# Kernel optimization log

Measured on AMD Instinct MI355X. Metric: run time of the kernel, lower is better.

Reference implementation:

```python
import jax, jax.numpy as jnp
import numpy as np

N = 100000   # nodes
E = 3200000  # edges (avg degree 32)
IN = 128     # in_channels
H = 128      # hidden_channels
G = 512      # graphs in batch


def setup_inputs() -> dict:
    key = jax.random.key(0)
    ks = jax.random.split(key, 8)
    x = jax.random.normal(ks[0], (N, IN), dtype=jnp.float32)
    edge_index = jax.random.randint(ks[1], (2, E), 0, N, dtype=jnp.int64)
    batch = jnp.sort(jax.random.randint(ks[2], (N,), 0, G, dtype=jnp.int64))
    s_in = 1.0 / np.sqrt(IN)
    s_h = 1.0 / np.sqrt(H)
    W1 = jax.random.normal(ks[3], (IN, H), dtype=jnp.float32) * s_in
    b1 = jnp.zeros((H,), dtype=jnp.float32)
    W2 = jax.random.normal(ks[4], (H, H), dtype=jnp.float32) * s_h
    b2 = jnp.zeros((H,), dtype=jnp.float32)
    Wc = jax.random.normal(ks[5], (H, 1), dtype=jnp.float32) * s_h
    bc = jnp.zeros((1,), dtype=jnp.float32)
    return {"x": x, "edge_index": edge_index, "batch": batch,
            "W1": W1, "b1": b1, "W2": W2, "b2": b2, "Wc": Wc, "bc": bc}


def _gcn_conv(x, W, b, src, dst, n):
    # PyG GCNConv: x' = D^{-1/2} (A+I) D^{-1/2} X W + b  (self-loops already in src/dst)
    h = x @ W                                      # [n, H] small GEMM
    ones = jnp.ones(src.shape[0], dtype=h.dtype)
    deg = jax.ops.segment_sum(ones, dst, num_segments=n)
    dinv = jnp.where(deg > 0, jax.lax.rsqrt(deg), 0.0)
    norm = dinv[src] * dinv[dst]                   # [E+n]
    msgs = h[src] * norm[:, None]                  # gather + scale (memory-bound)
    return jax.ops.segment_sum(msgs, dst, num_segments=n) + b


def reference(x, edge_index, batch, W1, b1, W2, b2, Wc, bc):
    n = x.shape[0]
    loop = jnp.arange(n, dtype=edge_index.dtype)
    src = jnp.concatenate([edge_index[0], loop])   # add self-loops
    dst = jnp.concatenate([edge_index[1], loop])
    h = jax.nn.relu(_gcn_conv(x, W1, b1, src, dst, n))
    h = jax.nn.relu(_gcn_conv(h, W2, b2, src, dst, n))
    # global_mean_pool: segment mean over graph ids
    counts = jax.ops.segment_sum(jnp.ones(n, dtype=h.dtype), batch, num_segments=G)
    sums = jax.ops.segment_sum(h, batch, num_segments=G)
    pooled = sums / jnp.maximum(counts, 1.0)[:, None]   # [G, H]
    return jax.nn.sigmoid(pooled @ Wc + bc)             # [G, 1]
```

## Files before the change

### kernel.cpp

```cpp
#include <hip/hip_runtime.h>

typedef unsigned short ushort_t;
typedef unsigned int uint_t;
typedef unsigned char u8_t;

typedef __bf16 bf16x8 __attribute__((ext_vector_type(8)));
typedef float f32x4 __attribute__((ext_vector_type(4)));
typedef uint_t uint32x4 __attribute__((ext_vector_type(4)));
typedef uint_t uint32x2 __attribute__((ext_vector_type(2)));
typedef _Float16 h2 __attribute__((ext_vector_type(2)));

#define EPB 20480
#define NSH 7
#define CAP 6144
#define BPAD 904

__device__ __forceinline__ float b2f(ushort_t u) {
    union { uint_t ui; float f; } c; c.ui = ((uint_t)u) << 16; return c.f;
}
__device__ __forceinline__ ushort_t f2b(float f) {
    union { float f; uint_t ui; } c; c.f = f;
    uint_t u = c.ui;
    uint_t r = (u + 0x7fffu + ((u >> 16) & 1u)) >> 16;
    return (ushort_t)r;
}
__device__ __forceinline__ u8_t f2e5(float x) {
    ushort_t h = __builtin_bit_cast(ushort_t, (_Float16)x);
    uint_t r = ((uint_t)h + 0x7Fu + ((h >> 8) & 1u)) >> 8;
    return (u8_t)r;
}
__device__ __forceinline__ void upk_add(uint_t d, h2* acc) {
    uint_t A = __builtin_amdgcn_perm(0u, d, 0x010C000Cu);
    uint_t B = __builtin_amdgcn_perm(0u, d, 0x030C020Cu);
    acc[0] += __builtin_bit_cast(h2, A);
    acc[1] += __builtin_bit_cast(h2, B);
}

__global__ __launch_bounds__(256) void p1_hist(const int* __restrict__ dst,
                                               int* __restrict__ H,
                                               const float* __restrict__ W1,
                                               const float* __restrict__ W2,
                                               ushort_t* __restrict__ W1t,
                                               ushort_t* __restrict__ W2t,
                                               u8_t* __restrict__ h8z,
                                               int E, int NBLK, int B, int N) {
    int t = threadIdx.x, c = blockIdx.x;
    if (c >= NBLK + 128) {
        if (t < 32) ((uint_t*)h8z)[(size_t)N * 32 + t] = 0u;
        return;
    }
    if (c >= NBLK) {
        int idx = (c - NBLK) * 256 + t;
        int sel = idx >> 14;
        int i = idx & 16383;
        int k = i >> 7, nn = i & 127;
        const float* S = sel ? W2 : W1;
        ushort_t* D = sel ? W2t : W1t;
        D[nn * 128 + k] = f2b(S[k * 128 + nn]);
        return;
    }
    __shared__ int hist[1024];
    for (int b = t; b < 1024; b += 256) hist[b] = 0;
    __syncthreads();
    int base = c * EPB;
    int lim = min(E - base, EPB);
    for (int i = t; i < lim; i += 256)
        atomicAdd(&hist[dst[base + i] >> NSH], 1);
    __syncthreads();
    for (int b = t; b < B; b += 256) H[b * NBLK + c] = hist[b];
}

__global__ __launch_bounds__(256) void reduce256(const int* __restrict__ in,
                                                 int* __restrict__ bsums, int n) {
    __shared__ int s[256];
    int t = threadIdx.x, g = blockIdx.x * 256 + t;
    s[t] = (g < n) ? in[g] : 0;
    __syncthreads();
    for (int o = 128; o > 0; o >>= 1) {
        if (t < o) s[t] += s[t + o];
        __syncthreads();
    }
    if (t == 0) bsums[blockIdx.x] = s[0];
}

__global__ __launch_bounds__(512) void scan_small(const int* __restrict__ in,
                                                  int* __restrict__ outEx, int n) {
    __shared__ int s[512];
    int t = threadIdx.x;
    int v = (t < n) ? in[t] : 0;
    s[t] = v;
    __syncthreads();
    for (int o = 1; o < 512; o <<= 1) {
        int x = 0;
        if (t >= o) x = s[t - o];
        __syncthreads();
        s[t] += x;
        __syncthreads();
    }
    if (t < n) outEx[t] = s[t] - v;
}

__global__ __launch_bounds__(256) void scan256ex(const int* __restrict__ in,
                                                 const int* __restrict__ boffs,
                                                 int* __restrict__ outEx, int n) {
    __shared__ int s[256];
    int t = threadIdx.x, g = blockIdx.x * 256 + t;
    int v = (g < n) ? in[g] : 0;
    s[t] = v;
    __syncthreads();
    for (int o = 1; o < 256; o <<= 1) {
        int x = 0;
        if (t >= o) x = s[t - o];
        __syncthreads();
        s[t] += x;
        __syncthreads();
    }
    if (g < n) outEx[g] = boffs[blockIdx.x] + s[t] - v;
}

__global__ __launch_bounds__(256) void p3_scatter(const int* __restrict__ src,
                                                  const int* __restrict__ dst,
                                                  const int* __restrict__ Hex,
                                                  uint_t* __restrict__ packed,
                                                  int E, int NBLK, int B) {
    __shared__ int offsL[1024];
    __shared__ int cur[1024];
    int t = threadIdx.x, c = blockIdx.x;
    for (int b = t; b < B; b += 256) {
        offsL[b] = Hex[b * NBLK + c];
        cur[b] = 0;
    }
    __syncthreads();
    int base = c * EPB;
    int lim = min(E - base, EPB);
    for (int i = t; i < lim; i += 256) {
        int d = dst[base + i];
        int s = src[base + i];
        int b = d >> NSH;
        int r = atomicAdd(&cur[b], 1);
        packed[offsL[b] + r] = ((uint_t)s << NSH) | (uint_t)(d & 127);
    }
}

__global__ __launch_bounds__(256) void p4_build(const uint_t* __restrict__ packed,
                                                const int* __restrict__ Hex,
                                                int* __restrict__ adj,
                                                int* __restrict__ offs,
                                                int* __restrict__ dgr,
                                                float* __restrict__ dinv,
                                                int E, int N, int NBLK, int B) {
    __shared__ uint_t ebuf[CAP];
    __shared__ uint_t sbuf[CAP];
    __shared__ int hist[1024];
    __shared__ int hbase[1024];
    __shared__ int psum[256];
    __shared__ int dcnt[128], loc[128], cur[128];
    __shared__ int pdg[128], ploc[128];
    int t = threadIdx.x, b = blockIdx.x;
    int bs = Hex[b * NBLK];
    int be = (b + 1 < B) ? Hex[(b + 1) * NBLK] : E;
    int m = be - bs;
    for (int i = t; i < 1024; i += 256) hist[i] = 0;
    if (t < 128) dcnt[t] = 0;
    __syncthreads();
    bool fits = (m <= CAP);
    for (int i = t; i < m; i += 256) {
        uint_t p = packed[bs + i];
        if (fits) ebuf[i] = p;
        atomicAdd(&dcnt[p & 127], 1);
        atomicAdd(&hist[p >> (2 * NSH)], 1);
    }
    __syncthreads();
    int v0 = hist[4 * t], v1 = hist[4 * t + 1], v2 = hist[4 * t + 2], v3 = hist[4 * t + 3];
    int tot = v0 + v1 + v2 + v3;
    psum[t] = tot;
    __syncthreads();
    for (int o = 1; o < 256; o <<= 1) {
        int x = 0;
        if (t >= o) x = psum[t - o];
        __syncthreads();
        psum[t] += x;
        __syncthreads();
    }
    int base = psum[t] - tot;
    hbase[4 * t]     = base;
    hbase[4 * t + 1] = base + v0;
    hbase[4 * t + 2] = base + v0 + v1;
    hbase[4 * t + 3] = base + v0 + v1 + v2;
    if (t < 128) {
        int pd = (dcnt[t] + 8) & ~7;
        pdg[t] = pd;
        ploc[t] = pd;
    }
    __syncthreads();
    for (int o = 1; o < 128; o <<= 1) {
        int x = 0;
        if (t < 128 && t >= o) x = ploc[t - o];
        __syncthreads();
        if (t < 128) ploc[t] += x;
        __syncthreads();
    }
    int bsp = ((bs + 7) & ~7) + b * BPAD;
    if (t < 128) {
        int ex = ploc[t] - pdg[t];
        int node = b * 128 + t;
        if (node < N) {
            int nbase = bsp + ex;
            offs[node] = nbase;
            dgr[node]  = pdg[t];
            dinv[node] = rsqrtf((float)(dcnt[t] + 1));
            adj[nbase] = node;
            for (int i = dcnt[t] + 1; i < pdg[t]; ++i)
                adj[nbase + i] = N;
        }
        loc[t] = ex + 1;
        cur[t] = 0;
    }
    __syncthreads();
    if (fits) {
        for (int i = t; i < m; i += 256) {
            uint_t p = ebuf[i];
            int r = atomicAdd(&hbase[p >> (2 * NSH)], 1);
            sbuf[r] = p;
        }
        __syncthreads();
        for (int i = t; i < m; i += 256) {
            uint_t p = sbuf[i];
            int l = p & 127;
            int r = atomicAdd(&cur[l], 1);
            adj[bsp + loc[l] + r] = (int)(p >> NSH);
        }
    } else {
        for (int i = t; i < m; i += 256) {
            uint_t p = packed[bs + i];
            int l = p & 127;
            int r = atomicAdd(&cur[l], 1);
            adj[bsp + loc[l] + r] = (int)(p >> NSH);
        }
    }
}

__global__ __launch_bounds__(256, 4) void gemm_scale(const ushort_t* __restrict__ Xin,
                                                     const ushort_t* __restrict__ Wt,
                                                     const float* __restrict__ dinv,
                                                     u8_t* __restrict__ Hout8, int n) {
    __shared__ ushort_t lds[128 * 136];
    int tid = threadIdx.x;
    for (int i = tid; i < 128 * 16; i += 256) {
        int r = i >> 4, c8 = (i & 15) << 3;
        *(uint32x4*)(lds + r * 136 + c8) = *(const uint32x4*)(Wt + r * 128 + c8);
    }
    __syncthreads();
    int lane = tid & 63, wave = tid >> 6;
    int m = lane & 15, q = lane >> 4;
    int row0 = blockIdx.x * 64 + wave * 16;
    int ar = row0 + m;
    if (ar > n - 1) ar = n - 1;
    bf16x8 a[4];
#pragma unroll
    for (int ks = 0; ks < 4; ++ks)
        a[ks] = __builtin_bit_cast(bf16x8,
            *(const uint32x4*)(Xin + (size_t)ar * 128 + ks * 32 + q * 8));
    f32x4 acc[8];
    f32x4 zero = {0.f, 0.f, 0.f, 0.f};
#pragma unroll
    for (int nt = 0; nt < 8; ++nt) acc[nt] = zero;
#pragma unroll
    for (int nt = 0; nt < 8; ++nt) {
#pragma unroll
        for (int ks = 0; ks < 4; ++ks) {
            bf16x8 b = __builtin_bit_cast(bf16x8,
                *(const uint32x4*)(lds + (nt * 16 + m) * 136 + ks * 32 + q * 8));
            acc[nt] = __builtin_amdgcn_mfma_f32_16x16x32_bf16(a[ks], b, acc[nt], 0, 0, 0);
        }
    }
    float dv[4];
#pragma unroll
    for (int r = 0; r < 4; ++r) {
        int gr = row0 + q * 4 + r;
        dv[r] = (gr < n) ? dinv[gr] : 0.f;
    }
#pragma unroll
    for (int nt = 0; nt < 8; ++nt) {
#pragma unroll
        for (int r = 0; r < 4; ++r) {
            int gr = row0 + q * 4 + r;
            if (gr < n)
                Hout8[(size_t)gr * 128 + nt * 16 + m] = f2e5(acc[nt][r] * dv[r]);
        }
    }
}

__global__ __launch_bounds__(256, 4) void gemm_scale_f32(const float* __restrict__ Xf,
                                                         const ushort_t* __restrict__ Wt,
                                                         const float* __restrict__ dinv,
                                                         u8_t* __restrict__ Hout8, int n) {
    __shared__ ushort_t lds[128 * 136];
    int tid = threadIdx.x;
    for (int i = tid; i < 128 * 16; i += 256) {
        int r = i >> 4, c8 = (i & 15) << 3;
        *(uint32x4*)(lds + r * 136 + c8) = *(const uint32x4*)(Wt + r * 128 + c8);
    }
    __syncthreads();
    int lane = tid & 63, wave = tid >> 6;
    int m = lane & 15, q = lane >> 4;
    int row0 = blockIdx.x * 64 + wave * 16;
    int ar = row0 + m;
    if (ar > n - 1) ar = n - 1;
    bf16x8 a[4];
#pragma unroll
    for (int ks = 0; ks < 4; ++ks) {
        const float* p = Xf + (size_t)ar * 128 + ks * 32 + q * 8;
        f32x4 lo = *(const f32x4*)p;
        f32x4 hi = *(const f32x4*)(p + 4);
        ushort_t t[8];
        t[0] = f2b(lo[0]); t[1] = f2b(lo[1]); t[2] = f2b(lo[2]); t[3] = f2b(lo[3]);
        t[4] = f2b(hi[0]); t[5] = f2b(hi[1]); t[6] = f2b(hi[2]); t[7] = f2b(hi[3]);
        a[ks] = __builtin_bit_cast(bf16x8, *(uint32x4*)t);
    }
    f32x4 acc[8];
    f32x4 zero = {0.f, 0.f, 0.f, 0.f};
#pragma unroll
    for (int nt = 0; nt < 8; ++nt) acc[nt] = zero;
#pragma unroll
    for (int nt = 0; nt < 8; ++nt) {
#pragma unroll
        for (int ks = 0; ks < 4; ++ks) {
            bf16x8 b = __builtin_bit_cast(bf16x8,
                *(const uint32x4*)(lds + (nt * 16 + m) * 136 + ks * 32 + q * 8));
            acc[nt] = __builtin_amdgcn_mfma_f32_16x16x32_bf16(a[ks], b, acc[nt], 0, 0, 0);
        }
    }
    float dv[4];
#pragma unroll
    for (int r = 0; r < 4; ++r) {
        int gr = row0 + q * 4 + r;
        dv[r] = (gr < n) ? dinv[gr] : 0.f;
    }
#pragma unroll
    for (int nt = 0; nt < 8; ++nt) {
#pragma unroll
        for (int r = 0; r < 4; ++r) {
            int gr = row0 + q * 4 + r;
            if (gr < n)
                Hout8[(size_t)gr * 128 + nt * 16 + m] = f2e5(acc[nt][r] * dv[r]);
        }
    }
}

__device__ __forceinline__ void agg_core(const u8_t* __restrict__ Hs8,
                                         const int* __restrict__ adj,
                                         int beg, int pd, int g, uint_t colb,
                                         h2* acc) {
    int e = 0;
    for (; e + 16 <= pd; e += 16) {
        const int4 sv = *(const int4*)(adj + beg + e + g * 4);
        uint_t o0 = ((uint_t)sv.x << 7) | colb;
        uint_t o1 = ((uint_t)sv.y << 7) | colb;
        uint_t o2 = ((uint_t)sv.z << 7) | colb;
        uint_t o3 = ((uint_t)sv.w << 7) | colb;
        uint32x2 w0 = *(const uint32x2*)(Hs8 + o0);
        uint32x2 w1 = *(const uint32x2*)(Hs8 + o1);
        uint32x2 w2 = *(const uint32x2*)(Hs8 + o2);
        uint32x2 w3 = *(const uint32x2*)(Hs8 + o3);
        upk_add(w0[0], acc); upk_add(w0[1], acc + 2);
        upk_add(w1[0], acc); upk_add(w1[1], acc + 2);
        upk_add(w2[0], acc); upk_add(w2[1], acc + 2);
        upk_add(w3[0], acc); upk_add(w3[1], acc + 2);
    }
    if (e < pd) {
        const int2 sv = *(const int2*)(adj + beg + e + g * 2);
        uint_t o0 = ((uint_t)sv.x << 7) | colb;
        uint_t o1 = ((uint_t)sv.y << 7) | colb;
        uint32x2 w0 = *(const uint32x2*)(Hs8 + o0);
        uint32x2 w1 = *(const uint32x2*)(Hs8 + o1);
        upk_add(w0[0], acc); upk_add(w0[1], acc + 2);
        upk_add(w1[0], acc); upk_add(w1[1], acc + 2);
    }
}

__device__ __forceinline__ void slot_reduce(h2* acc) {
#pragma unroll
    for (int k = 0; k < 4; ++k) {
        uint_t v = __builtin_bit_cast(uint_t, acc[k]);
        acc[k] += __builtin_bit_cast(h2, (uint_t)__shfl_xor(v, 16, 64));
        v = __builtin_bit_cast(uint_t, acc[k]);
        acc[k] += __builtin_bit_cast(h2, (uint_t)__shfl_xor(v, 32, 64));
    }
}

__global__ __launch_bounds__(256, 4) void agg_kernel(const u8_t* __restrict__ Hs8,
                                                     const int* __restrict__ adj,
                                                     const int* __restrict__ offs,
                                                     const int* __restrict__ dgr,
                                                     const float* __restrict__ dinv,
                                                     const float* __restrict__ bias,
                                                     ushort_t* __restrict__ Out, int n) {
    int node = blockIdx.x * 4 + (threadIdx.x >> 6);
    if (node >= n) return;
    int lane = threadIdx.x & 63;
    int g = lane >> 4;
    int l16 = lane & 15;
    uint_t colb = (uint_t)l16 * 8;
    const int beg = offs[node];
    const int pd  = dgr[node];
    h2 acc[4];
    h2 hz = {(_Float16)0.f, (_Float16)0.f};
#pragma unroll
    for (int k = 0; k < 4; ++k) acc[k] = hz;
    agg_core(Hs8, adj, beg, pd, g, colb, acc);
    slot_reduce(acc);
    if (g == 0) {
        float di = dinv[node];
        ushort_t o[8];
#pragma unroll
        for (int k = 0; k < 4; ++k) {
            float f0 = (float)acc[k][0];
            float f1 = (float)acc[k][1];
            o[2 * k]     = f2b(fmaxf(di * f0 + bias[colb + 2 * k], 0.f));
            o[2 * k + 1] = f2b(fmaxf(di * f1 + bias[colb + 2 * k + 1], 0.f));
        }
        *(uint32x4*)(Out + (size_t)node * 128 + colb) = *(uint32x4*)o;
    }
}

__global__ __launch_bounds__(256, 4) void agg_pool_kernel(const u8_t* __restrict__ Hs8,
                                                          const int* __restrict__ adj,
                                                          const int* __restrict__ offs,
                                                          const int* __restrict__ dgr,
                                                          const float* __restrict__ dinv,
                                                          const float* __restrict__ bias,
                                                          const float* __restrict__ Wc,
                                                          float* __restrict__ Sout, int n) {
    int node = blockIdx.x * 4 + (threadIdx.x >> 6);
    if (node >= n) return;
    int lane = threadIdx.x & 63;
    int g = lane >> 4;
    int l16 = lane & 15;
    uint_t colb = (uint_t)l16 * 8;
    const int beg = offs[node];
    const int pd  = dgr[node];
    h2 acc[4];
    h2 hz = {(_Float16)0.f, (_Float16)0.f};
#pragma unroll
    for (int k = 0; k < 4; ++k) acc[k] = hz;
    agg_core(Hs8, adj, beg, pd, g, colb, acc);
    slot_reduce(acc);
    float local = 0.f;
    float di = dinv[node];
#pragma unroll
    for (int k = 0; k < 4; ++k) {
        float f0 = fmaxf(di * (float)acc[k][0] + bias[colb + 2 * k], 0.f);
        float f1 = fmaxf(di * (float)acc[k][1] + bias[colb + 2 * k + 1], 0.f);
        local += f0 * Wc[colb + 2 * k] + f1 * Wc[colb + 2 * k + 1];
    }
    local += __shfl_xor(local, 1, 64);
    local += __shfl_xor(local, 2, 64);
    local += __shfl_xor(local, 4, 64);
    local += __shfl_xor(local, 8, 64);
    if (lane == 0) Sout[node] = local;
}

__global__ __launch_bounds__(256) void pool2_kernel(const float* __restrict__ S,
                                                    const int* __restrict__ batch,
                                                    const float* __restrict__ bc,
                                                    float* __restrict__ out, int n) {
    int g = blockIdx.x;
    int t = threadIdx.x;
    int lo = 0, hi = n;
    while (lo < hi) { int mid = (lo + hi) >> 1; if (batch[mid] < g) lo = mid + 1; else hi = mid; }
    int start = lo;
    hi = n;
    while (lo < hi) { int mid = (lo + hi) >> 1; if (batch[mid] < g + 1) lo = mid + 1; else hi = mid; }
    int stop = lo;
    float s = 0.f;
    for (int i = start + t; i < stop; i += 256) s += S[i];
    __shared__ float red[256];
    red[t] = s;
    __syncthreads();
    for (int o = 128; o > 0; o >>= 1) {
        if (t < o) red[t] += red[t + o];
        __syncthreads();
    }
    if (t == 0) {
        int cg = stop - start;
        float z = red[0] / (float)(cg > 0 ? cg : 1) + bc[0];
        out[g] = 1.f / (1.f + expf(-z));
    }
}

extern "C" void kernel_launch(void* const* d_in, const int* in_sizes, int n_in,
                              void* d_out, int out_size, void* d_ws, size_t ws_size,
                              hipStream_t stream) {
    const float* X     = (const float*)d_in[0];
    const int* ei      = (const int*)d_in[1];
    const int* batch   = (const int*)d_in[2];
    const float* W1    = (const float*)d_in[3];
    const float* b1    = (const float*)d_in[4];
    const float* W2    = (const float*)d_in[5];
    const float* b2    = (const float*)d_in[6];
    const float* Wc    = (const float*)d_in[7];
    const float* bc    = (const float*)d_in[8];

    const int N = in_sizes[2];
    const int E = in_sizes[1] / 2;
    const int G = out_size;
    const int* srcv = ei;
    const int* dstv = ei + E;

    const int NBLK = (E + EPB - 1) / EPB;
    const int B    = (N + 127) >> NSH;
    const int n0   = B * NBLK;
    const int g1   = (n0 + 255) / 256;

    char* p = (char*)d_ws;
    auto alloc = [&](size_t bytes) -> void* {
        void* r = (void*)p;
        p += (bytes + 255) & ~(size_t)255;
        return r;
    };
    int* H         = (int*)alloc((size_t)n0 * 4);
    int* Hex       = (int*)alloc((size_t)n0 * 4);
    int* S1        = (int*)alloc((size_t)g1 * 4);
    int* S1ex      = (int*)alloc((size_t)g1 * 4);
    uint_t* packed = (uint_t*)alloc((size_t)E * 4);
    int* adj       = (int*)alloc(((size_t)E + (size_t)B * BPAD + 128) * 4);
    int* offs      = (int*)alloc(((size_t)N + 1) * 4);
    int* dgr       = (int*)alloc((size_t)N * 4);
    float* dinv    = (float*)alloc((size_t)N * 4);
    ushort_t* W1t  = (ushort_t*)alloc(16384 * 2);
    ushort_t* W2t  = (ushort_t*)alloc(16384 * 2);
    u8_t* h8       = (u8_t*)alloc(((size_t)N + 1) * 128);
    ushort_t* bufA = (ushort_t*)alloc((size_t)N * 128 * 2);
    float* Snode   = (float*)alloc((size_t)N * 4);

    p1_hist<<<NBLK + 129, 256, 0, stream>>>(dstv, H, W1, W2, W1t, W2t, h8, E, NBLK, B, N);
    reduce256<<<g1, 256, 0, stream>>>(H, S1, n0);
    scan_small<<<1, 512, 0, stream>>>(S1, S1ex, g1);
    scan256ex<<<g1, 256, 0, stream>>>(H, S1ex, Hex, n0);
    p3_scatter<<<NBLK, 256, 0, stream>>>(srcv, dstv, Hex, packed, E, NBLK, B);
    p4_build<<<B, 256, 0, stream>>>(packed, Hex, adj, offs, dgr, dinv, E, N, NBLK, B);

    const int GB = (N + 63) / 64;
    const int AB = (N + 3) / 4;
    gemm_scale_f32<<<GB, 256, 0, stream>>>(X, W1t, dinv, h8, N);
    agg_kernel<<<AB, 256, 0, stream>>>(h8, adj, offs, dgr, dinv, b1, bufA, N);
    gemm_scale<<<GB, 256, 0, stream>>>(bufA, W2t, dinv, h8, N);
    agg_pool_kernel<<<AB, 256, 0, stream>>>(h8, adj, offs, dgr, dinv, b2, Wc, Snode, N);
    pool2_kernel<<<G, 256, 0, stream>>>(Snode, batch, bc, (float*)d_out, N);
}
```

Before: 370.2 us.

## Split FP8 feature table into four 32-column chunks for cache-local aggregation

Stores the 8-bit node feature table as four column-major chunks of 32 columns each. Aggregation kernels launch one grid pass per chunk, so each gather hits a quarter-size table that fits better in cache. Each wave now uses 8 edge slots of 8 lanes instead of 4 of 16, and the pooling stage sums four partial node scores. The cost is reading the adjacency four times and issuing smaller 4-byte gathers, plus extra shuffle reductions.

```diff
diff --git a/kernel.cpp b/kernel.cpp
--- a/kernel.cpp
+++ b/kernel.cpp
@@ -14,6 +14,7 @@
 #define NSH 7
 #define CAP 6144
 #define BPAD 904
+#define NCHUNK 4
 
 __device__ __forceinline__ float b2f(ushort_t u) {
     union { uint_t ui; float f; } c; c.ui = ((uint_t)u) << 16; return c.f;
@@ -46,7 +47,11 @@
                                                int E, int NBLK, int B, int N) {
     int t = threadIdx.x, c = blockIdx.x;
     if (c >= NBLK + 128) {
-        if (t < 32) ((uint_t*)h8z)[(size_t)N * 32 + t] = 0u;
+        if (t < 32) {
+            int ch = t >> 3, d = t & 7;
+            size_t s32 = (size_t)(N + 1) * 32;
+            ((uint_t*)(h8z + (size_t)ch * s32 + (size_t)N * 32))[d] = 0u;
+        }
         return;
     }
     if (c >= NBLK) {
@@ -280,13 +285,16 @@
         int gr = row0 + q * 4 + r;
         dv[r] = (gr < n) ? dinv[gr] : 0.f;
     }
+    size_t s32 = (size_t)(n + 1) * 32;
 #pragma unroll
     for (int nt = 0; nt < 8; ++nt) {
+        int col = nt * 16 + m;
+        u8_t* cbase = Hout8 + (size_t)(col >> 5) * s32 + (col & 31);
 #pragma unroll
         for (int r = 0; r < 4; ++r) {
             int gr = row0 + q * 4 + r;
             if (gr < n)
-                Hout8[(size_t)gr * 128 + nt * 16 + m] = f2e5(acc[nt][r] * dv[r]);
+                cbase[(size_t)gr * 32] = f2e5(acc[nt][r] * dv[r]);
         }
     }
 }
@@ -337,128 +345,137 @@
         int gr = row0 + q * 4 + r;
         dv[r] = (gr < n) ? dinv[gr] : 0.f;
     }
+    size_t s32 = (size_t)(n + 1) * 32;
 #pragma unroll
     for (int nt = 0; nt < 8; ++nt) {
+        int col = nt * 16 + m;
+        u8_t* cbase = Hout8 + (size_t)(col >> 5) * s32 + (col & 31);
 #pragma unroll
         for (int r = 0; r < 4; ++r) {
             int gr = row0 + q * 4 + r;
             if (gr < n)
-                Hout8[(size_t)gr * 128 + nt * 16 + m] = f2e5(acc[nt][r] * dv[r]);
-        }
-    }
-}
-
-__device__ __forceinline__ void agg_core(const u8_t* __restrict__ Hs8,
-                                         const int* __restrict__ adj,
-                                         int beg, int pd, int g, uint_t colb,
-                                         h2* acc) {
+                cbase[(size_t)gr * 32] = f2e5(acc[nt][r] * dv[r]);
+        }
+    }
+}
+
+__device__ __forceinline__ void agg_core32(const u8_t* __restrict__ cb,
+                                           const int* __restrict__ adj,
+                                           int beg, int pd, int slot, uint_t colb,
+                                           h2* acc) {
     int e = 0;
-    for (; e + 16 <= pd; e += 16) {
-        const int4 sv = *(const int4*)(adj + beg + e + g * 4);
-        uint_t o0 = ((uint_t)sv.x << 7) | colb;
-        uint_t o1 = ((uint_t)sv.y << 7) | colb;
-        uint_t o2 = ((uint_t)sv.z << 7) | colb;
-        uint_t o3 = ((uint_t)sv.w << 7) | colb;
-        uint32x2 w0 = *(const uint32x2*)(Hs8 + o0);
-        uint32x2 w1 = *(const uint32x2*)(Hs8 + o1);
-        uint32x2 w2 = *(const uint32x2*)(Hs8 + o2);
-        uint32x2 w3 = *(const uint32x2*)(Hs8 + o3);
-        upk_add(w0[0], acc); upk_add(w0[1], acc + 2);
-        upk_add(w1[0], acc); upk_add(w1[1], acc + 2);
-        upk_add(w2[0], acc); upk_add(w2[1], acc + 2);
-        upk_add(w3[0], acc); upk_add(w3[1], acc + 2);
+    for (; e + 32 <= pd; e += 32) {
+        const int4 sv = *(const int4*)(adj + beg + e + slot * 4);
+        uint_t w0 = *(const uint_t*)(cb + ((((uint_t)sv.x) << 5) | colb));
+        uint_t w1 = *(const uint_t*)(cb + ((((uint_t)sv.y) << 5) | colb));
+        uint_t w2 = *(const uint_t*)(cb + ((((uint_t)sv.z) << 5) | colb));
+        uint_t w3 = *(const uint_t*)(cb + ((((uint_t)sv.w) << 5) | colb));
+        upk_add(w0, acc); upk_add(w1, acc);
+        upk_add(w2, acc); upk_add(w3, acc);
+    }
+    if (e + 16 <= pd) {
+        const int2 sv = *(const int2*)(adj + beg + e + slot * 2);
+        uint_t w0 = *(const uint_t*)(cb + ((((uint_t)sv.x) << 5) | colb));
+        uint_t w1 = *(const uint_t*)(cb + ((((uint_t)sv.y) << 5) | colb));
+        upk_add(w0, acc); upk_add(w1, acc);
+        e += 16;
     }
     if (e < pd) {
-        const int2 sv = *(const int2*)(adj + beg + e + g * 2);
-        uint_t o0 = ((uint_t)sv.x << 7) | colb;
-        uint_t o1 = ((uint_t)sv.y << 7) | colb;
-        uint32x2 w0 = *(const uint32x2*)(Hs8 + o0);
-        uint32x2 w1 = *(const uint32x2*)(Hs8 + o1);
-        upk_add(w0[0], acc); upk_add(w0[1], acc + 2);
-        upk_add(w1[0], acc); upk_add(w1[1], acc + 2);
-    }
-}
-
-__device__ __forceinline__ void slot_reduce(h2* acc) {
-#pragma unroll
-    for (int k = 0; k < 4; ++k) {
+        int s = adj[beg + e + slot];
+        uint_t w = *(const uint_t*)(cb + ((((uint_t)s) << 5) | colb));
+        upk_add(w, acc);
+    }
+}
+
+__device__ __forceinline__ void slot_reduce32(h2* acc) {
+#pragma unroll
+    for (int k = 0; k < 2; ++k) {
         uint_t v = __builtin_bit_cast(uint_t, acc[k]);
+        acc[k] += __builtin_bit_cast(h2, (uint_t)__shfl_xor(v, 8, 64));
+        v = __builtin_bit_cast(uint_t, acc[k]);
         acc[k] += __builtin_bit_cast(h2, (uint_t)__shfl_xor(v, 16, 64));
         v = __builtin_bit_cast(uint_t, acc[k]);
         acc[k] += __builtin_bit_cast(h2, (uint_t)__shfl_xor(v, 32, 64));
     }
 }
 
-__global__ __launch_bounds__(256, 4) void agg_kernel(const u8_t* __restrict__ Hs8,
+__global__ __launch_bounds__(256, 8) void agg_kernel(const u8_t* __restrict__ Hs8,
                                                      const int* __restrict__ adj,
                                                      const int* __restrict__ offs,
                                                      const int* __restrict__ dgr,
                                                      const float* __restrict__ dinv,
                                                      const float* __restrict__ bias,
-                                                     ushort_t* __restrict__ Out, int n) {
-    int node = blockIdx.x * 4 + (threadIdx.x >> 6);
+                                                     ushort_t* __restrict__ Out,
+                                                     int n, int AB) {
+    int chunk = blockIdx.x / AB;
+    int nb = blockIdx.x - chunk * AB;
+    int node = nb * 4 + (threadIdx.x >> 6);
     if (node >= n) return;
     int lane = threadIdx.x & 63;
-    int g = lane >> 4;
-    int l16 = lane & 15;
-    uint_t colb = (uint_t)l16 * 8;
+    int slot = lane >> 3;
+    int l8 = lane & 7;
+    uint_t colb = (uint_t)l8 * 4;
+    const u8_t* cb = Hs8 + (size_t)chunk * ((size_t)(n + 1) * 32);
     const int beg = offs[node];
     const int pd  = dgr[node];
-    h2 acc[4];
+    h2 acc[2];
     h2 hz = {(_Float16)0.f, (_Float16)0.f};
-#pragma unroll
-    for (int k = 0; k < 4; ++k) acc[k] = hz;
-    agg_core(Hs8, adj, beg, pd, g, colb, acc);
-    slot_reduce(acc);
-    if (g == 0) {
+    acc[0] = hz; acc[1] = hz;
+    agg_core32(cb, adj, beg, pd, slot, colb, acc);
+    slot_reduce32(acc);
+    if (slot == 0) {
         float di = dinv[node];
-        ushort_t o[8];
-#pragma unroll
-        for (int k = 0; k < 4; ++k) {
+        int cbase = chunk * 32 + l8 * 4;
+        ushort_t o[4];
+#pragma unroll
+        for (int k = 0; k < 2; ++k) {
             float f0 = (float)acc[k][0];
             float f1 = (float)acc[k][1];
-            o[2 * k]     = f2b(fmaxf(di * f0 + bias[colb + 2 * k], 0.f));
-            o[2 * k + 1] = f2b(fmaxf(di * f1 + bias[colb + 2 * k + 1], 0.f));
-        }
-        *(uint32x4*)(Out + (size_t)node * 128 + colb) = *(uint32x4*)o;
-    }
-}
-
-__global__ __launch_bounds__(256, 4) void agg_pool_kernel(const u8_t* __restrict__ Hs8,
+            o[2 * k]     = f2b(fmaxf(di * f0 + bias[cbase + 2 * k], 0.f));
+            o[2 * k + 1] = f2b(fmaxf(di * f1 + bias[cbase + 2 * k + 1], 0.f));
+        }
+        *(uint32x2*)(Out + (size_t)node * 128 + cbase) = *(uint32x2*)o;
+    }
+}
+
+__global__ __launch_bounds__(256, 8) void agg_pool_kernel(const u8_t* __restrict__ Hs8,
                                                           const int* __restrict__ adj,
                                                           const int* __restrict__ offs,
                                                           const int* __restrict__ dgr,
                                                           const float* __restrict__ dinv,
                                                           const float* __restrict__ bias,
                                                           const float* __restrict__ Wc,
-                                                          float* __restrict__ Sout, int n) {
-    int node = blockIdx.x * 4 + (threadIdx.x >> 6);
+                                                          float* __restrict__ Sout,
+                                                          int n, int AB) {
+    int chunk = blockIdx.x / AB;
+    int nb = blockIdx.x - chunk * AB;
+    int node = nb * 4 + (threadIdx.x >> 6);
     if (node >= n) return;
     int lane = threadIdx.x & 63;
-    int g = lane >> 4;
-    int l16 = lane & 15;
-    uint_t colb = (uint_t)l16 * 8;
+    int slot = lane >> 3;
+    int l8 = lane & 7;
+    uint_t colb = (uint_t)l8 * 4;
+    const u8_t* cb = Hs8 + (size_t)chunk * ((size_t)(n + 1) * 32);
     const int beg = offs[node];
     const int pd  = dgr[node];
-    h2 acc[4];
+    h2 acc[2];
     h2 hz = {(_Float16)0.f, (_Float16)0.f};
-#pragma unroll
-    for (int k = 0; k < 4; ++k) acc[k] = hz;
-    agg_core(Hs8, adj, beg, pd, g, colb, acc);
-    slot_reduce(acc);
+    acc[0] = hz; acc[1] = hz;
+    agg_core32(cb, adj, beg, pd, slot, colb, acc);
+    slot_reduce32(acc);
+    float di = dinv[node];
+    int cbase = chunk * 32 + l8 * 4;
     float local = 0.f;
-    float di = dinv[node];
-#pragma unroll
-    for (int k = 0; k < 4; ++k) {
-        float f0 = fmaxf(di * (float)acc[k][0] + bias[colb + 2 * k], 0.f);
-        float f1 = fmaxf(di * (float)acc[k][1] + bias[colb + 2 * k + 1], 0.f);
-        local += f0 * Wc[colb + 2 * k] + f1 * Wc[colb + 2 * k + 1];
+#pragma unroll
+    for (int k = 0; k < 2; ++k) {
+        float f0 = fmaxf(di * (float)acc[k][0] + bias[cbase + 2 * k], 0.f);
+        float f1 = fmaxf(di * (float)acc[k][1] + bias[cbase + 2 * k + 1], 0.f);
+        local += f0 * Wc[cbase + 2 * k] + f1 * Wc[cbase + 2 * k + 1];
     }
     local += __shfl_xor(local, 1, 64);
     local += __shfl_xor(local, 2, 64);
     local += __shfl_xor(local, 4, 64);
-    local += __shfl_xor(local, 8, 64);
-    if (lane == 0) Sout[node] = local;
+    if (lane == 0) Sout[(size_t)chunk * n + node] = local;
 }
 
 __global__ __launch_bounds__(256) void pool2_kernel(const float* __restrict__ S,
@@ -474,7 +491,8 @@
     while (lo < hi) { int mid = (lo + hi) >> 1; if (batch[mid] < g + 1) lo = mid + 1; else hi = mid; }
     int stop = lo;
     float s = 0.f;
-    for (int i = start + t; i < stop; i += 256) s += S[i];
+    for (int i = start + t; i < stop; i += 256)
+        s += S[i] + S[(size_t)n + i] + S[2 * (size_t)n + i] + S[3 * (size_t)n + i];
     __shared__ float red[256];
     red[t] = s;
     __syncthreads();
@@ -532,7 +550,7 @@
     ushort_t* W2t  = (ushort_t*)alloc(16384 * 2);
     u8_t* h8       = (u8_t*)alloc(((size_t)N + 1) * 128);
     ushort_t* bufA = (ushort_t*)alloc((size_t)N * 128 * 2);
-    float* Snode   = (float*)alloc((size_t)N * 4);
+    float* Snode   = (float*)alloc((size_t)NCHUNK * N * 4);
 
     p1_hist<<<NBLK + 129, 256, 0, stream>>>(dstv, H, W1, W2, W1t, W2t, h8, E, NBLK, B, N);
     reduce256<<<g1, 256, 0, stream>>>(H, S1, n0);
@@ -544,8 +562,9 @@
     const int GB = (N + 63) / 64;
     const int AB = (N + 3) / 4;
     gemm_scale_f32<<<GB, 256, 0, stream>>>(X, W1t, dinv, h8, N);
-    agg_kernel<<<AB, 256, 0, stream>>>(h8, adj, offs, dgr, dinv, b1, bufA, N);
+    agg_kernel<<<NCHUNK * AB, 256, 0, stream>>>(h8, adj, offs, dgr, dinv, b1, bufA, N, AB);
     gemm_scale<<<GB, 256, 0, stream>>>(bufA, W2t, dinv, h8, N);
-    agg_pool_kernel<<<AB, 256, 0, stream>>>(h8, adj, offs, dgr, dinv, b2, Wc, Snode, N);
+    agg_pool_kernel<<<NCHUNK * AB, 256, 0, stream>>>(h8, adj, offs, dgr, dinv, b2, Wc,
+                                                     Snode, N, AB);
     pool2_kernel<<<G, 256, 0, stream>>>(Snode, batch, bc, (float*)d_out, N);
 }
```

New measurement: 524.1 us. 1.42x slower.

## Replace two-level bucketed CSR build with global-atomic degree count and scatter

Applied to the files above, without the earlier changes.

Replaces the bucketed histogram, packed-scatter and per-bucket LDS sort CSR construction with a simpler pipeline: global atomic degree counting, a node-level scan that writes offsets, dinv, self-loop and padding, then a global-atomic scatter of sources into adjacency. This removes the packed intermediate array and the LDS-heavy build kernel. In exchange it relies on contended global atomics over 100k counters and loses the src-sorted order within each node's neighbour list, which may hurt gather locality in aggregation.

```diff
diff --git a/kernel.cpp b/kernel.cpp
--- a/kernel.cpp
+++ b/kernel.cpp
@@ -10,11 +10,6 @@
 typedef uint_t uint32x2 __attribute__((ext_vector_type(2)));
 typedef _Float16 h2 __attribute__((ext_vector_type(2)));
 
-#define EPB 20480
-#define NSH 7
-#define CAP 6144
-#define BPAD 904
-
 __device__ __forceinline__ float b2f(ushort_t u) {
     union { uint_t ui; float f; } c; c.ui = ((uint_t)u) << 16; return c.f;
 }
@@ -36,21 +31,16 @@
     acc[1] += __builtin_bit_cast(h2, B);
 }
 
-__global__ __launch_bounds__(256) void p1_hist(const int* __restrict__ dst,
-                                               int* __restrict__ H,
-                                               const float* __restrict__ W1,
-                                               const float* __restrict__ W2,
-                                               ushort_t* __restrict__ W1t,
-                                               ushort_t* __restrict__ W2t,
-                                               u8_t* __restrict__ h8z,
-                                               int E, int NBLK, int B, int N) {
+__global__ __launch_bounds__(256) void k_init(const float* __restrict__ W1,
+                                              const float* __restrict__ W2,
+                                              ushort_t* __restrict__ W1t,
+                                              ushort_t* __restrict__ W2t,
+                                              u8_t* __restrict__ h8z,
+                                              int* __restrict__ deg,
+                                              int* __restrict__ cur, int N) {
     int t = threadIdx.x, c = blockIdx.x;
-    if (c >= NBLK + 128) {
-        if (t < 32) ((uint_t*)h8z)[(size_t)N * 32 + t] = 0u;
-        return;
-    }
-    if (c >= NBLK) {
-        int idx = (c - NBLK) * 256 + t;
+    if (c < 128) {
+        int idx = c * 256 + t;
         int sel = idx >> 14;
         int i = idx & 16383;
         int k = i >> 7, nn = i & 127;
@@ -59,22 +49,27 @@
         D[nn * 128 + k] = f2b(S[k * 128 + nn]);
         return;
     }
-    __shared__ int hist[1024];
-    for (int b = t; b < 1024; b += 256) hist[b] = 0;
-    __syncthreads();
-    int base = c * EPB;
-    int lim = min(E - base, EPB);
-    for (int i = t; i < lim; i += 256)
-        atomicAdd(&hist[dst[base + i] >> NSH], 1);
-    __syncthreads();
-    for (int b = t; b < B; b += 256) H[b * NBLK + c] = hist[b];
-}
-
-__global__ __launch_bounds__(256) void reduce256(const int* __restrict__ in,
+    if (c == 128) {
+        if (t < 32) ((uint_t*)h8z)[(size_t)N * 32 + t] = 0u;
+        return;
+    }
+    int i = (c - 129) * 256 + t;
+    if (i < N) deg[i] = 0;
+    else if (i < 2 * N) cur[i - N] = 0;
+}
+
+__global__ __launch_bounds__(256) void k_deg(const int* __restrict__ dst,
+                                             int* __restrict__ deg, int E) {
+    int stride = gridDim.x * 256;
+    for (int i = blockIdx.x * 256 + threadIdx.x; i < E; i += stride)
+        atomicAdd(&deg[dst[i]], 1);
+}
+
+__global__ __launch_bounds__(256) void reduce_pd(const int* __restrict__ deg,
                                                  int* __restrict__ bsums, int n) {
     __shared__ int s[256];
     int t = threadIdx.x, g = blockIdx.x * 256 + t;
-    s[t] = (g < n) ? in[g] : 0;
+    s[t] = (g < n) ? ((deg[g] + 8) & ~7) : 0;
     __syncthreads();
     for (int o = 128; o > 0; o >>= 1) {
         if (t < o) s[t] += s[t + o];
@@ -100,12 +95,18 @@
     if (t < n) outEx[t] = s[t] - v;
 }
 
-__global__ __launch_bounds__(256) void scan256ex(const int* __restrict__ in,
-                                                 const int* __restrict__ boffs,
-                                                 int* __restrict__ outEx, int n) {
+__global__ __launch_bounds__(256) void scan_nodes(const int* __restrict__ deg,
+                                                  const int* __restrict__ boffs,
+                                                  int* __restrict__ adj,
+                                                  int* __restrict__ offs,
+                                                  int* __restrict__ dgr,
+                                                  float* __restrict__ dinv,
+                                                  int n, int N) {
     __shared__ int s[256];
     int t = threadIdx.x, g = blockIdx.x * 256 + t;
-    int v = (g < n) ? in[g] : 0;
+    int d = (g < n) ? deg[g] : 0;
+    int pd = (d + 8) & ~7;
+    int v = (g < n) ? pd : 0;
     s[t] = v;
     __syncthreads();
     for (int o = 1; o < 256; o <<= 1) {
@@ -115,128 +116,28 @@
         s[t] += x;
         __syncthreads();
     }
-    if (g < n) outEx[g] = boffs[blockIdx.x] + s[t] - v;
-}
-
-__global__ __launch_bounds__(256) void p3_scatter(const int* __restrict__ src,
-                                                  const int* __restrict__ dst,
-                                                  const int* __restrict__ Hex,
-                                                  uint_t* __restrict__ packed,
-                                                  int E, int NBLK, int B) {
-    __shared__ int offsL[1024];
-    __shared__ int cur[1024];
-    int t = threadIdx.x, c = blockIdx.x;
-    for (int b = t; b < B; b += 256) {
-        offsL[b] = Hex[b * NBLK + c];
-        cur[b] = 0;
-    }
-    __syncthreads();
-    int base = c * EPB;
-    int lim = min(E - base, EPB);
-    for (int i = t; i < lim; i += 256) {
-        int d = dst[base + i];
-        int s = src[base + i];
-        int b = d >> NSH;
-        int r = atomicAdd(&cur[b], 1);
-        packed[offsL[b] + r] = ((uint_t)s << NSH) | (uint_t)(d & 127);
-    }
-}
-
-__global__ __launch_bounds__(256) void p4_build(const uint_t* __restrict__ packed,
-                                                const int* __restrict__ Hex,
-                                                int* __restrict__ adj,
-                                                int* __restrict__ offs,
-                                                int* __restrict__ dgr,
-                                                float* __restrict__ dinv,
-                                                int E, int N, int NBLK, int B) {
-    __shared__ uint_t ebuf[CAP];
-    __shared__ uint_t sbuf[CAP];
-    __shared__ int hist[1024];
-    __shared__ int hbase[1024];
-    __shared__ int psum[256];
-    __shared__ int dcnt[128], loc[128], cur[128];
-    __shared__ int pdg[128], ploc[128];
-    int t = threadIdx.x, b = blockIdx.x;
-    int bs = Hex[b * NBLK];
-    int be = (b + 1 < B) ? Hex[(b + 1) * NBLK] : E;
-    int m = be - bs;
-    for (int i = t; i < 1024; i += 256) hist[i] = 0;
-    if (t < 128) dcnt[t] = 0;
-    __syncthreads();
-    bool fits = (m <= CAP);
-    for (int i = t; i < m; i += 256) {
-        uint_t p = packed[bs + i];
-        if (fits) ebuf[i] = p;
-        atomicAdd(&dcnt[p & 127], 1);
-        atomicAdd(&hist[p >> (2 * NSH)], 1);
-    }
-    __syncthreads();
-    int v0 = hist[4 * t], v1 = hist[4 * t + 1], v2 = hist[4 * t + 2], v3 = hist[4 * t + 3];
-    int tot = v0 + v1 + v2 + v3;
-    psum[t] = tot;
-    __syncthreads();
-    for (int o = 1; o < 256; o <<= 1) {
-        int x = 0;
-        if (t >= o) x = psum[t - o];
-        __syncthreads();
-        psum[t] += x;
-        __syncthreads();
-    }
-    int base = psum[t] - tot;
-    hbase[4 * t]     = base;
-    hbase[4 * t + 1] = base + v0;
-    hbase[4 * t + 2] = base + v0 + v1;
-    hbase[4 * t + 3] = base + v0 + v1 + v2;
-    if (t < 128) {
-        int pd = (dcnt[t] + 8) & ~7;
-        pdg[t] = pd;
-        ploc[t] = pd;
-    }
-    __syncthreads();
-    for (int o = 1; o < 128; o <<= 1) {
-        int x = 0;
-        if (t < 128 && t >= o) x = ploc[t - o];
-        __syncthreads();
-        if (t < 128) ploc[t] += x;
-        __syncthreads();
-    }
-    int bsp = ((bs + 7) & ~7) + b * BPAD;
-    if (t < 128) {
-        int ex = ploc[t] - pdg[t];
-        int node = b * 128 + t;
-        if (node < N) {
-            int nbase = bsp + ex;
-            offs[node] = nbase;
-            dgr[node]  = pdg[t];
-            dinv[node] = rsqrtf((float)(dcnt[t] + 1));
-            adj[nbase] = node;
-            for (int i = dcnt[t] + 1; i < pdg[t]; ++i)
-                adj[nbase + i] = N;
-        }
-        loc[t] = ex + 1;
-        cur[t] = 0;
-    }
-    __syncthreads();
-    if (fits) {
-        for (int i = t; i < m; i += 256) {
-            uint_t p = ebuf[i];
-            int r = atomicAdd(&hbase[p >> (2 * NSH)], 1);
-            sbuf[r] = p;
-        }
-        __syncthreads();
-        for (int i = t; i < m; i += 256) {
-            uint_t p = sbuf[i];
-            int l = p & 127;
-            int r = atomicAdd(&cur[l], 1);
-            adj[bsp + loc[l] + r] = (int)(p >> NSH);
-        }
-    } else {
-        for (int i = t; i < m; i += 256) {
-            uint_t p = packed[bs + i];
-            int l = p & 127;
-            int r = atomicAdd(&cur[l], 1);
-            adj[bsp + loc[l] + r] = (int)(p >> NSH);
-        }
+    if (g < n) {
+        int base = boffs[blockIdx.x] + s[t] - v;
+        offs[g] = base;
+        dgr[g]  = pd;
+        dinv[g] = rsqrtf((float)(d + 1));
+        adj[base] = g;
+        for (int i = d + 1; i < pd; ++i)
+            adj[base + i] = N;
+    }
+}
+
+__global__ __launch_bounds__(256) void k_scatter(const int* __restrict__ src,
+                                                 const int* __restrict__ dst,
+                                                 const int* __restrict__ offs,
+                                                 int* __restrict__ cur,
+                                                 int* __restrict__ adj, int E) {
+    int stride = gridDim.x * 256;
+    for (int i = blockIdx.x * 256 + threadIdx.x; i < E; i += stride) {
+        int d = dst[i];
+        int s = src[i];
+        int r = atomicAdd(&cur[d], 1);
+        adj[offs[d] + 1 + r] = s;
     }
 }
 
@@ -508,10 +409,8 @@
     const int* srcv = ei;
     const int* dstv = ei + E;
 
-    const int NBLK = (E + EPB - 1) / EPB;
-    const int B    = (N + 127) >> NSH;
-    const int n0   = B * NBLK;
-    const int g1   = (n0 + 255) / 256;
+    const int g1 = (N + 255) / 256;
+    const int ZB = (2 * N + 255) / 256;
 
     char* p = (char*)d_ws;
     auto alloc = [&](size_t bytes) -> void* {
@@ -519,27 +418,26 @@
         p += (bytes + 255) & ~(size_t)255;
         return r;
     };
-    int* H         = (int*)alloc((size_t)n0 * 4);
-    int* Hex       = (int*)alloc((size_t)n0 * 4);
-    int* S1        = (int*)alloc((size_t)g1 * 4);
-    int* S1ex      = (int*)alloc((size_t)g1 * 4);
-    uint_t* packed = (uint_t*)alloc((size_t)E * 4);
-    int* adj       = (int*)alloc(((size_t)E + (size_t)B * BPAD + 128) * 4);
+    int* deg       = (int*)alloc((size_t)N * 4);
+    int* cur       = (int*)alloc((size_t)N * 4);
+    int* adj       = (int*)alloc(((size_t)E + 8 * (size_t)N + 64) * 4);
     int* offs      = (int*)alloc(((size_t)N + 1) * 4);
     int* dgr       = (int*)alloc((size_t)N * 4);
     float* dinv    = (float*)alloc((size_t)N * 4);
+    int* S1        = (int*)alloc((size_t)g1 * 4);
+    int* S1ex      = (int*)alloc((size_t)g1 * 4);
     ushort_t* W1t  = (ushort_t*)alloc(16384 * 2);
     ushort_t* W2t  = (ushort_t*)alloc(16384 * 2);
     u8_t* h8       = (u8_t*)alloc(((size_t)N + 1) * 128);
     ushort_t* bufA = (ushort_t*)alloc((size_t)N * 128 * 2);
     float* Snode   = (float*)alloc((size_t)N * 4);
 
-    p1_hist<<<NBLK + 129, 256, 0, stream>>>(dstv, H, W1, W2, W1t, W2t, h8, E, NBLK, B, N);
-    reduce256<<<g1, 256, 0, stream>>>(H, S1, n0);
+    k_init<<<129 + ZB, 256, 0, stream>>>(W1, W2, W1t, W2t, h8, deg, cur, N);
+    k_deg<<<1024, 256, 0, stream>>>(dstv, deg, E);
+    reduce_pd<<<g1, 256, 0, stream>>>(deg, S1, N);
     scan_small<<<1, 512, 0, stream>>>(S1, S1ex, g1);
-    scan256ex<<<g1, 256, 0, stream>>>(H, S1ex, Hex, n0);
-    p3_scatter<<<NBLK, 256, 0, stream>>>(srcv, dstv, Hex, packed, E, NBLK, B);
-    p4_build<<<B, 256, 0, stream>>>(packed, Hex, adj, offs, dgr, dinv, E, N, NBLK, B);
+    scan_nodes<<<g1, 256, 0, stream>>>(deg, S1ex, adj, offs, dgr, dinv, N, N);
+    k_scatter<<<1024, 256, 0, stream>>>(srcv, dstv, offs, cur, adj, E);
 
     const int GB = (N + 63) / 64;
     const int AB = (N + 3) / 4;
```

Result: slower. 606.9 us (+63.9%).
